# Optimization experiments

Hardware: AMD Instinct MI355X
Metric: run time of the kernel (lower is better)

## Reference

```python
import jax, jax.numpy as jnp
import numpy as np
import math

B, S, D, H, FF = 8, 1024, 1024, 16, 4096
DH = D // H
EPS = 1e-5


def _layernorm(x, g, b):
    mu = jnp.mean(x, axis=-1, keepdims=True)
    var = jnp.mean((x - mu) ** 2, axis=-1, keepdims=True)
    return (x - mu) * jax.lax.rsqrt(var + EPS) * g + b


def _gelu_tanh(x):
    c = math.sqrt(2.0 / math.pi)
    return 0.5 * x * (1.0 + jnp.tanh(c * (x + 0.044715 * x ** 3)))


def setup_inputs() -> dict:
    key = jax.random.key(0)
    ks = jax.random.split(key, 8)
    s = lambda d: 1.0 / math.sqrt(d)
    return {
        "x": jax.random.normal(ks[0], (B, S, D), jnp.float32),
        "ln1_g": jnp.ones((D,), jnp.float32),
        "ln1_b": jnp.zeros((D,), jnp.float32),
        "w_qkv": jax.random.normal(ks[1], (3 * D, D), jnp.float32) * s(D),
        "b_qkv": jax.random.normal(ks[2], (3 * D,), jnp.float32) * 0.02,
        "w_o": jax.random.normal(ks[3], (D, D), jnp.float32) * s(D),
        "b_o": jax.random.normal(ks[4], (D,), jnp.float32) * 0.02,
        "ln2_g": jnp.ones((D,), jnp.float32),
        "ln2_b": jnp.zeros((D,), jnp.float32),
        "w1": jax.random.normal(ks[5], (FF, D), jnp.float32) * s(D),
        "b1": jax.random.normal(ks[6], (FF,), jnp.float32) * 0.02,
        "w2": jax.random.normal(ks[7], (D, FF), jnp.float32) * s(FF),
        "b2": jnp.zeros((D,), jnp.float32),
    }


def reference(x, ln1_g, ln1_b, w_qkv, b_qkv, w_o, b_o, ln2_g, ln2_b, w1, b1, w2, b2):
    # --- pre-LN causal self-attention ---
    h = _layernorm(x, ln1_g, ln1_b)
    qkv = h @ w_qkv.T + b_qkv                      # [B,S,3D]
    q, k, v = jnp.split(qkv, 3, axis=-1)
    q = q.reshape(B, S, H, DH)
    k = k.reshape(B, S, H, DH)
    v = v.reshape(B, S, H, DH)
    scores = jnp.einsum("bqhd,bkhd->bhqk", q, k) / math.sqrt(DH)
    causal = jnp.triu(jnp.ones((S, S), jnp.bool_), 1)  # True above diagonal
    scores = jnp.where(causal, -jnp.inf, scores)
    attn = jax.nn.softmax(scores, axis=-1)
    o = jnp.einsum("bhqk,bkhd->bqhd", attn, v).reshape(B, S, D)
    x = x + (o @ w_o.T + b_o)
    # --- FFN ---
    h = _layernorm(x, ln2_g, ln2_b)
    h = _gelu_tanh(h @ w1.T + b1) @ w2.T + b2
    return x + h
```

## Files before the change

kernel.cpp:

```cpp
#include <hip/hip_runtime.h>
#include <math.h>


typedef __bf16 bf16_t;
typedef __bf16 bf16x4 __attribute__((ext_vector_type(4)));
typedef __bf16 bf16x8 __attribute__((ext_vector_type(8)));
typedef float f32x4 __attribute__((ext_vector_type(4)));

#define WAITVM(N) asm volatile("s_waitcnt vmcnt(" #N ")" ::: "memory")

__device__ __forceinline__ void async16(const void* g, void* l) {
    __builtin_amdgcn_global_load_lds(
        (const __attribute__((address_space(1))) void*)g,
        (__attribute__((address_space(3))) void*)l,
        16, 0, 0);
}

__device__ __forceinline__ void ln_row(const float* __restrict__ x,
                                       const float* __restrict__ g,
                                       const float* __restrict__ bb,
                                       bf16_t* __restrict__ out, int row) {
    const int tid = threadIdx.x;
    const float4 xv = *(const float4*)(x + row * 1024 + tid * 4);
    float s1 = xv.x + xv.y + xv.z + xv.w;
    float s2 = xv.x * xv.x + xv.y * xv.y + xv.z * xv.z + xv.w * xv.w;
#pragma unroll
    for (int m = 32; m >= 1; m >>= 1) {
        s1 += __shfl_xor(s1, m);
        s2 += __shfl_xor(s2, m);
    }
    __shared__ float r1[4], r2[4];
    const int wid = tid >> 6, lane = tid & 63;
    if (lane == 0) { r1[wid] = s1; r2[wid] = s2; }
    __syncthreads();
    s1 = r1[0] + r1[1] + r1[2] + r1[3];
    s2 = r2[0] + r2[1] + r2[2] + r2[3];
    const float mu = s1 * (1.0f / 1024.0f);
    const float var = s2 * (1.0f / 1024.0f) - mu * mu;
    const float rs = rsqrtf(var + 1e-5f);
    const float4 gv = *(const float4*)(g + tid * 4);
    const float4 bv = *(const float4*)(bb + tid * 4);
    bf16x4 o;
    o[0] = (bf16_t)((xv.x - mu) * rs * gv.x + bv.x);
    o[1] = (bf16_t)((xv.y - mu) * rs * gv.y + bv.y);
    o[2] = (bf16_t)((xv.z - mu) * rs * gv.z + bv.z);
    o[3] = (bf16_t)((xv.w - mu) * rs * gv.w + bv.w);
    *(bf16x4*)(out + row * 1024 + tid * 4) = o;
}

__global__ __launch_bounds__(256) void prep(
    const float* __restrict__ s0, const float* __restrict__ s1,
    const float* __restrict__ s2, const float* __restrict__ s3,
    bf16_t* __restrict__ d0, bf16_t* __restrict__ d1,
    bf16_t* __restrict__ d2, bf16_t* __restrict__ d3,
    const float* __restrict__ x, const float* __restrict__ ln1g,
    const float* __restrict__ ln1b, bf16_t* __restrict__ h) {
    if (blockIdx.x >= 12288) {
        ln_row(x, ln1g, ln1b, h, blockIdx.x - 12288);
        return;
    }
    const int g = blockIdx.x * 256 + threadIdx.x;
    const float* s;
    bf16_t* d;
    int off;
    if (g < 786432)       { s = s0; d = d0; off = g; }
    else if (g < 1048576) { s = s1; d = d1; off = g - 786432; }
    else if (g < 2097152) { s = s2; d = d2; off = g - 1048576; }
    else                  { s = s3; d = d3; off = g - 2097152; }
    const int i = off * 4;
    const float4 v = *(const float4*)(s + i);
    bf16x4 o;
    o[0] = (bf16_t)v.x; o[1] = (bf16_t)v.y; o[2] = (bf16_t)v.z; o[3] = (bf16_t)v.w;
    *(bf16x4*)(d + i) = o;
}

__global__ __launch_bounds__(256) void ln_b(const bf16_t* __restrict__ x,
                                            const float* __restrict__ g,
                                            const float* __restrict__ bb,
                                            bf16_t* __restrict__ out) {
    const int tid = threadIdx.x;
    const int row = blockIdx.x;
    const bf16x4 xb = *(const bf16x4*)(x + row * 1024 + tid * 4);
    const float x0 = (float)xb[0], x1 = (float)xb[1], x2 = (float)xb[2], x3 = (float)xb[3];
    float s1 = x0 + x1 + x2 + x3;
    float s2 = x0 * x0 + x1 * x1 + x2 * x2 + x3 * x3;
#pragma unroll
    for (int m = 32; m >= 1; m >>= 1) {
        s1 += __shfl_xor(s1, m);
        s2 += __shfl_xor(s2, m);
    }
    __shared__ float r1[4], r2[4];
    const int wid = tid >> 6, lane = tid & 63;
    if (lane == 0) { r1[wid] = s1; r2[wid] = s2; }
    __syncthreads();
    s1 = r1[0] + r1[1] + r1[2] + r1[3];
    s2 = r2[0] + r2[1] + r2[2] + r2[3];
    const float mu = s1 * (1.0f / 1024.0f);
    const float var = s2 * (1.0f / 1024.0f) - mu * mu;
    const float rs = rsqrtf(var + 1e-5f);
    const float4 gv = *(const float4*)(g + tid * 4);
    const float4 bv = *(const float4*)(bb + tid * 4);
    bf16x4 o;
    o[0] = (bf16_t)((x0 - mu) * rs * gv.x + bv.x);
    o[1] = (bf16_t)((x1 - mu) * rs * gv.y + bv.y);
    o[2] = (bf16_t)((x2 - mu) * rs * gv.z + bv.z);
    o[3] = (bf16_t)((x3 - mu) * rs * gv.w + bv.w);
    *(bf16x4*)(out + row * 1024 + tid * 4) = o;
}

template <int MODE>
__global__ __launch_bounds__(256, 2) void gemm_bt(
    const bf16_t* __restrict__ A, const bf16_t* __restrict__ W,
    const float* __restrict__ bias, const float* __restrict__ residf,
    const bf16_t* __restrict__ residb,
    bf16_t* __restrict__ outb, float* __restrict__ outf,
    bf16_t* __restrict__ vt, int N, int K) {
    __shared__ bf16_t As[128 * 64];
    __shared__ bf16_t Bs[128 * 64];
    const int tid = threadIdx.x;
    const int w = tid >> 6;
    const int lane = tid & 63;
    const int l15 = lane & 15;
    const int quad = lane >> 4;

    const int nbn = N >> 7;
    const int per = 8 * nbn;
    const int lid = blockIdx.x;
    const int bm = (lid / per) * 8 + (lid % per) % 8;
    const int bn = (lid % per) / 8;
    const int m0 = bm * 128;
    const int n0 = bn * 128;
    const int wm = (w & 1) * 64;
    const int wn = (w >> 1) * 64;

    int rr[4], so[4];
#pragma unroll
    for (int q = 0; q < 4; q++) {
        const int c = q * 256 + w * 64 + lane;
        rr[q] = c >> 3;
        so[q] = ((c & 7) ^ (rr[q] & 7)) * 8;
    }
    const bf16_t* pA[4];
    const bf16_t* pB[4];
#pragma unroll
    for (int q = 0; q < 4; q++) {
        pA[q] = A + (size_t)(m0 + rr[q]) * K + so[q];
        pB[q] = W + (size_t)(n0 + rr[q]) * K + so[q];
    }

    f32x4 acc[4][4] = {};

    for (int k0 = 0; k0 < K; k0 += 64) {
#pragma unroll
        for (int q = 0; q < 4; q++) {
            async16(pA[q], As + q * 2048 + w * 512);
            async16(pB[q], Bs + q * 2048 + w * 512);
            pA[q] += 64; pB[q] += 64;
        }
        __syncthreads();

        bf16x8 af[4][2], bfr[4][2];
#pragma unroll
        for (int i = 0; i < 4; i++) {
            const int r = wm + i * 16 + l15;
#pragma unroll
            for (int f = 0; f < 2; f++) {
                const int slot = (f * 4 + quad) ^ (r & 7);
                af[i][f] = *(const bf16x8*)(As + r * 64 + slot * 8);
            }
        }
#pragma unroll
        for (int j = 0; j < 4; j++) {
            const int r = wn + j * 16 + l15;
#pragma unroll
            for (int f = 0; f < 2; f++) {
                const int slot = (f * 4 + quad) ^ (r & 7);
                bfr[j][f] = *(const bf16x8*)(Bs + r * 64 + slot * 8);
            }
        }
#pragma unroll
        for (int i = 0; i < 4; i++)
#pragma unroll
            for (int j = 0; j < 4; j++)
#pragma unroll
                for (int f = 0; f < 2; f++)
                    acc[i][j] = __builtin_amdgcn_mfma_f32_16x16x32_bf16(
                        af[i][f], bfr[j][f], acc[i][j], 0, 0, 0);
        __syncthreads();
    }

#pragma unroll
    for (int i = 0; i < 4; i++) {
#pragma unroll
        for (int j = 0; j < 4; j++) {
            const int col = n0 + wn + j * 16 + l15;
            const float bcol = bias[col];
            const int row0 = m0 + wm + i * 16 + quad * 4;
            float v4[4];
#pragma unroll
            for (int q = 0; q < 4; q++) {
                float v = acc[i][j][q] + bcol;
                if (MODE == 1) {
                    const float u2 = -1.5957691216057308f * (v + 0.044715f * v * v * v);
                    v = v * __builtin_amdgcn_rcpf(1.0f + __expf(u2));
                }
                v4[q] = v;
            }
            if (MODE == 4) {
#pragma unroll
                for (int q = 0; q < 4; q++) {
                    const size_t idx = (size_t)(row0 + q) * N + col;
                    outb[idx] = (bf16_t)(v4[q] + residf[idx]);
                }
            } else if (MODE == 5) {
#pragma unroll
                for (int q = 0; q < 4; q++) {
                    const size_t idx = (size_t)(row0 + q) * N + col;
                    outf[idx] = v4[q] + (float)residb[idx];
                }
            } else if (MODE == 3 && col >= 2048) {
                const int bh = (row0 >> 10) * 16 + ((col - 2048) >> 6);
                const int d = (col - 2048) & 63;
                bf16x4 pk;
#pragma unroll
                for (int q = 0; q < 4; q++) pk[q] = (bf16_t)v4[q];
                *(bf16x4*)(vt + (size_t)bh * 65536 + d * 1024 + (row0 & 1023)) = pk;
            } else {
#pragma unroll
                for (int q = 0; q < 4; q++)
                    outb[(size_t)(row0 + q) * N + col] = (bf16_t)v4[q];
            }
        }
    }
}

template <int MODE>
__global__ __launch_bounds__(512, 2) void gemm8(
    const bf16_t* __restrict__ A, const bf16_t* __restrict__ W,
    const float* __restrict__ bias, bf16_t* __restrict__ outb,
    bf16_t* __restrict__ vt, int N, int K) {
    __shared__ bf16_t lds[65536];
    const int tid = threadIdx.x;
    const int w = tid >> 6, lane = tid & 63;
    const int l15 = lane & 15, quad = lane >> 4;
    const int wr = w >> 2, wc = w & 3;

    const int nbn = N >> 8;
    const int per = 8 * nbn;
    const int lid = blockIdx.x;
    const int bm = (lid / per) * 8 + (lid % per) % 8;
    const int bn = (lid % per) / 8;
    const int m0 = bm << 8, n0 = bn << 8;

    int r_[2], s_[2];
#pragma unroll
    for (int L = 0; L < 2; L++) {
        const int c = L * 512 + tid;
        r_[L] = c >> 3;
        s_[L] = ((c & 7) ^ (r_[L] & 7)) * 8;
    }
    const bf16_t* pa0[2]; const bf16_t* pa1[2];
    const bf16_t* pb0[2]; const bf16_t* pb1[2];
#pragma unroll
    for (int L = 0; L < 2; L++) {
        pa0[L] = A + (size_t)(m0 + r_[L]) * K + s_[L];
        pa1[L] = pa0[L] + (size_t)128 * K;
        pb0[L] = W + (size_t)(n0 + r_[L]) * K + s_[L];
        pb1[L] = pb0[L] + (size_t)128 * K;
    }

    int ra[8], rb[4];
#pragma unroll
    for (int i = 0; i < 8; i++) ra[i] = (i >> 2) * 128 + wr * 64 + (i & 3) * 16 + l15;
#pragma unroll
    for (int j = 0; j < 4; j++) rb[j] = (j >> 1) * 128 + wc * 32 + (j & 1) * 16 + l15;

#define FRAG(base, row, f) \
    (*(const bf16x8*)((base) + (row) * 64 + ((((f) * 4 + quad) ^ ((row) & 7)) * 8)))

    f32x4 acc[8][4] = {};
    bf16x8 af[4][2], bfr[4][2];

    async16(pa0[0], lds + w * 512);
    async16(pa0[1], lds + 4096 + w * 512);
    async16(pb0[0], lds + 16384 + w * 512);
    async16(pb0[1], lds + 16384 + 4096 + w * 512);
    async16(pb1[0], lds + 16384 + 8192 + w * 512);
    async16(pb1[1], lds + 16384 + 8192 + 4096 + w * 512);
    async16(pa1[0], lds + 8192 + w * 512);
    async16(pa1[1], lds + 8192 + 4096 + w * 512);

    const int NT = K >> 6;
    int p = 0;
    for (int t = 0; t < NT - 1; ++t, p ^= 1) {
        const bf16_t* Ab = lds + p * 32768;
        const bf16_t* Bb = Ab + 16384;
        const int q2 = p ^ 1;
        const int kn = (t + 1) << 6;
        WAITVM(4);
        __builtin_amdgcn_s_barrier();
#pragma unroll
        for (int i = 0; i < 4; i++) { af[i][0] = FRAG(Ab, ra[i], 0); af[i][1] = FRAG(Ab, ra[i], 1); }
#pragma unroll
        for (int j = 0; j < 2; j++) { bfr[j][0] = FRAG(Bb, rb[j], 0); bfr[j][1] = FRAG(Bb, rb[j], 1); }
        async16(pa0[0] + kn, lds + q2 * 32768 + w * 512);
        async16(pa0[1] + kn, lds + q2 * 32768 + 4096 + w * 512);
        __builtin_amdgcn_s_setprio(1);
#pragma unroll
        for (int i = 0; i < 4; i++)
#pragma unroll
            for (int j = 0; j < 2; j++)
#pragma unroll
                for (int f = 0; f < 2; f++)
                    acc[i][j] = __builtin_amdgcn_mfma_f32_16x16x32_bf16(af[i][f], bfr[j][f], acc[i][j], 0, 0, 0);
        __builtin_amdgcn_s_setprio(0);
        __builtin_amdgcn_s_barrier();
        WAITVM(4);
        __builtin_amdgcn_s_barrier();
#pragma unroll
        for (int j = 2; j < 4; j++) { bfr[j][0] = FRAG(Bb, rb[j], 0); bfr[j][1] = FRAG(Bb, rb[j], 1); }
        async16(pb0[0] + kn, lds + q2 * 32768 + 16384 + w * 512);
        async16(pb0[1] + kn, lds + q2 * 32768 + 16384 + 4096 + w * 512);
        __builtin_amdgcn_s_setprio(1);
#pragma unroll
        for (int i = 0; i < 4; i++)
#pragma unroll
            for (int j = 2; j < 4; j++)
#pragma unroll
                for (int f = 0; f < 2; f++)
                    acc[i][j] = __builtin_amdgcn_mfma_f32_16x16x32_bf16(af[i][f], bfr[j][f], acc[i][j], 0, 0, 0);
        __builtin_amdgcn_s_setprio(0);
        __builtin_amdgcn_s_barrier();
        WAITVM(4);
        __builtin_amdgcn_s_barrier();
#pragma unroll
        for (int i = 0; i < 4; i++) { af[i][0] = FRAG(Ab, ra[i + 4], 0); af[i][1] = FRAG(Ab, ra[i + 4], 1); }
        async16(pb1[0] + kn, lds + q2 * 32768 + 16384 + 8192 + w * 512);
        async16(pb1[1] + kn, lds + q2 * 32768 + 16384 + 8192 + 4096 + w * 512);
        __builtin_amdgcn_s_setprio(1);
#pragma unroll
        for (int i = 0; i < 4; i++)
#pragma unroll
            for (int j = 0; j < 2; j++)
#pragma unroll
                for (int f = 0; f < 2; f++)
                    acc[i + 4][j] = __builtin_amdgcn_mfma_f32_16x16x32_bf16(af[i][f], bfr[j][f], acc[i + 4][j], 0, 0, 0);
        __builtin_amdgcn_s_setprio(0);
        __builtin_amdgcn_s_barrier();
        async16(pa1[0] + kn, lds + q2 * 32768 + 8192 + w * 512);
        async16(pa1[1] + kn, lds + q2 * 32768 + 8192 + 4096 + w * 512);
        __builtin_amdgcn_s_setprio(1);
#pragma unroll
        for (int i = 0; i < 4; i++)
#pragma unroll
            for (int j = 2; j < 4; j++)
#pragma unroll
                for (int f = 0; f < 2; f++)
                    acc[i + 4][j] = __builtin_amdgcn_mfma_f32_16x16x32_bf16(af[i][f], bfr[j][f], acc[i + 4][j], 0, 0, 0);
        __builtin_amdgcn_s_setprio(0);
        __builtin_amdgcn_s_barrier();
    }
    {
        const bf16_t* Ab = lds + p * 32768;
        const bf16_t* Bb = Ab + 16384;
        WAITVM(4);
        __builtin_amdgcn_s_barrier();
#pragma unroll
        for (int i = 0; i < 4; i++) { af[i][0] = FRAG(Ab, ra[i], 0); af[i][1] = FRAG(Ab, ra[i], 1); }
#pragma unroll
        for (int j = 0; j < 2; j++) { bfr[j][0] = FRAG(Bb, rb[j], 0); bfr[j][1] = FRAG(Bb, rb[j], 1); }
        __builtin_amdgcn_s_setprio(1);
#pragma unroll
        for (int i = 0; i < 4; i++)
#pragma unroll
            for (int j = 0; j < 2; j++)
#pragma unroll
                for (int f = 0; f < 2; f++)
                    acc[i][j] = __builtin_amdgcn_mfma_f32_16x16x32_bf16(af[i][f], bfr[j][f], acc[i][j], 0, 0, 0);
        __builtin_amdgcn_s_setprio(0);
        __builtin_amdgcn_s_barrier();
        WAITVM(2);
        __builtin_amdgcn_s_barrier();
#pragma unroll
        for (int j = 2; j < 4; j++) { bfr[j][0] = FRAG(Bb, rb[j], 0); bfr[j][1] = FRAG(Bb, rb[j], 1); }
        __builtin_amdgcn_s_setprio(1);
#pragma unroll
        for (int i = 0; i < 4; i++)
#pragma unroll
            for (int j = 2; j < 4; j++)
#pragma unroll
                for (int f = 0; f < 2; f++)
                    acc[i][j] = __builtin_amdgcn_mfma_f32_16x16x32_bf16(af[i][f], bfr[j][f], acc[i][j], 0, 0, 0);
        __builtin_amdgcn_s_setprio(0);
        __builtin_amdgcn_s_barrier();
        WAITVM(0);
        __builtin_amdgcn_s_barrier();
#pragma unroll
        for (int i = 0; i < 4; i++) { af[i][0] = FRAG(Ab, ra[i + 4], 0); af[i][1] = FRAG(Ab, ra[i + 4], 1); }
        __builtin_amdgcn_s_setprio(1);
#pragma unroll
        for (int i = 0; i < 4; i++)
#pragma unroll
            for (int j = 0; j < 2; j++)
#pragma unroll
                for (int f = 0; f < 2; f++)
                    acc[i + 4][j] = __builtin_amdgcn_mfma_f32_16x16x32_bf16(af[i][f], bfr[j][f], acc[i + 4][j], 0, 0, 0);
#pragma unroll
        for (int i = 0; i < 4; i++)
#pragma unroll
            for (int j = 2; j < 4; j++)
#pragma unroll
                for (int f = 0; f < 2; f++)
                    acc[i + 4][j] = __builtin_amdgcn_mfma_f32_16x16x32_bf16(af[i][f], bfr[j][f], acc[i + 4][j], 0, 0, 0);
        __builtin_amdgcn_s_setprio(0);
    }
#undef FRAG

#pragma unroll
    for (int i = 0; i < 8; i++) {
        const int row0 = m0 + (i >> 2) * 128 + wr * 64 + (i & 3) * 16 + quad * 4;
#pragma unroll
        for (int j = 0; j < 4; j++) {
            const int col = n0 + (j >> 1) * 128 + wc * 32 + (j & 1) * 16 + l15;
            const float bcol = bias[col];
            float v4[4];
#pragma unroll
            for (int q = 0; q < 4; q++) {
                float v = acc[i][j][q] + bcol;
                if (MODE == 1) {
                    const float u2 = -1.5957691216057308f * (v + 0.044715f * v * v * v);
                    v = v * __builtin_amdgcn_rcpf(1.0f + __expf(u2));
                }
                v4[q] = v;
            }
            if (MODE == 3 && col >= 2048) {
                const int bh = (row0 >> 10) * 16 + ((col - 2048) >> 6);
                const int d = (col - 2048) & 63;
                bf16x4 pk;
#pragma unroll
                for (int q = 0; q < 4; q++) pk[q] = (bf16_t)v4[q];
                *(bf16x4*)(vt + (size_t)bh * 65536 + d * 1024 + (row0 & 1023)) = pk;
            } else {
#pragma unroll
                for (int q = 0; q < 4; q++)
                    outb[(size_t)(row0 + q) * N + col] = (bf16_t)v4[q];
            }
        }
    }
}

__global__ __launch_bounds__(512) void attn_mfma(const bf16_t* __restrict__ qkv,
                                                 const bf16_t* __restrict__ vt,
                                                 bf16_t* __restrict__ o) {
    __shared__ bf16_t Ks[4096];
    __shared__ bf16_t Vs[4096];
    __shared__ bf16_t Ps[8][32][72];
    const int tid = threadIdx.x;
    const int w = tid >> 6;
    const int lane = tid & 63;
    const int l15 = lane & 15;
    const int quad = lane >> 4;
    const int qb = blockIdx.x;
    const int bh = blockIdx.y;
    const int b = bh >> 4, h = bh & 15;

    const int qrow = b * 1024 + qb * 256 + w * 32;

    bf16x8 qf[2][2];
#pragma unroll
    for (int g = 0; g < 2; g++)
#pragma unroll
        for (int f = 0; f < 2; f++) {
            bf16x8 t = *(const bf16x8*)(qkv + (size_t)(qrow + g * 16 + l15) * 3072 + h * 64 + f * 32 + quad * 8);
#pragma unroll
            for (int e = 0; e < 8; e++) t[e] = (bf16_t)((float)t[e] * 0.125f);
            qf[g][f] = t;
        }

    f32x4 Ot[2][4] = {};
    float mrow[2] = {-3.0e38f, -3.0e38f};
    float lrow[2] = {0.0f, 0.0f};

    const int c0 = w * 64 + lane;
    const int r0 = c0 >> 3, g0 = (((c0 & 7) ^ (r0 & 7))) * 8;

    const bf16_t* kbase = qkv + (size_t)(b * 1024) * 3072 + 1024 + h * 64;
    const bf16_t* vbase = vt + (size_t)bh * 64 * 1024;

    const int ktmax = 4 * qb + 3;
    for (int kt = 0; kt <= ktmax; kt++) {
        async16(kbase + (size_t)(kt * 64 + r0) * 3072 + g0, Ks + w * 512);
        async16(vbase + (size_t)r0 * 1024 + kt * 64 + g0, Vs + w * 512);
        __syncthreads();

#pragma unroll
        for (int g = 0; g < 2; g++) {
            const int qmaxw = qb * 256 + w * 32 + g * 16 + 15;
            if (kt * 64 > qmaxw) continue;
            const int ktd = qmaxw >> 6;
            const int kbd = (2 * w + g) & 3;

            f32x4 sf[4];
#pragma unroll
            for (int kb = 0; kb < 4; kb++) {
                if (kt * 64 + kb * 16 > qmaxw) {
                    sf[kb] = (f32x4){-3.0e38f, -3.0e38f, -3.0e38f, -3.0e38f};
                    continue;
                }
                const int r = kb * 16 + l15;
                f32x4 acc = {};
#pragma unroll
                for (int f = 0; f < 2; f++) {
                    const int seg = (f * 4 + quad) ^ (r & 7);
                    const bf16x8 kf = *(const bf16x8*)(Ks + r * 64 + seg * 8);
                    acc = __builtin_amdgcn_mfma_f32_16x16x32_bf16(kf, qf[g][f], acc, 0, 0, 0);
                }
                if (kt == ktd && kb == kbd) {
#pragma unroll
                    for (int rr2 = 0; rr2 < 4; rr2++)
                        if (quad * 4 + rr2 > l15) acc[rr2] = -3.0e38f;
                }
                sf[kb] = acc;
            }

            float tmax = -3.0e38f;
#pragma unroll
            for (int kb = 0; kb < 4; kb++)
#pragma unroll
                for (int rr2 = 0; rr2 < 4; rr2++) tmax = fmaxf(tmax, sf[kb][rr2]);
            tmax = fmaxf(tmax, __shfl_xor(tmax, 16));
            tmax = fmaxf(tmax, __shfl_xor(tmax, 32));
            const float mnew = fmaxf(mrow[g], tmax);
            const float alpha = __expf(mrow[g] - mnew);
            float psum = 0.0f;
#pragma unroll
            for (int kb = 0; kb < 4; kb++) {
                bf16x4 pk;
#pragma unroll
                for (int rr2 = 0; rr2 < 4; rr2++) {
                    const float p = __expf(sf[kb][rr2] - mnew);
                    psum += p;
                    pk[rr2] = (bf16_t)p;
                }
                *(bf16x4*)(&Ps[w][g * 16 + l15][kb * 16 + quad * 4]) = pk;
            }
            psum += __shfl_xor(psum, 16);
            psum += __shfl_xor(psum, 32);
            lrow[g] = lrow[g] * alpha + psum;
            mrow[g] = mnew;
#pragma unroll
            for (int db = 0; db < 4; db++)
#pragma unroll
                for (int rr2 = 0; rr2 < 4; rr2++) Ot[g][db][rr2] *= alpha;

#pragma unroll
            for (int ks = 0; ks < 2; ks++) {
                if (kt * 64 + ks * 32 > qmaxw) break;
                const bf16x8 pf = *(const bf16x8*)(&Ps[w][g * 16 + l15][ks * 32 + quad * 8]);
#pragma unroll
                for (int db = 0; db < 4; db++) {
                    const int d = db * 16 + l15;
                    const int seg = (ks * 4 + quad) ^ (d & 7);
                    const bf16x8 vf = *(const bf16x8*)(Vs + d * 64 + seg * 8);
                    Ot[g][db] = __builtin_amdgcn_mfma_f32_16x16x32_bf16(vf, pf, Ot[g][db], 0, 0, 0);
                }
            }
        }
        __syncthreads();
    }

#pragma unroll
    for (int g = 0; g < 2; g++) {
        const float rl = 1.0f / lrow[g];
#pragma unroll
        for (int db = 0; db < 4; db++) {
            bf16x4 ov;
#pragma unroll
            for (int rr2 = 0; rr2 < 4; rr2++) ov[rr2] = (bf16_t)(Ot[g][db][rr2] * rl);
            *(bf16x4*)(o + (size_t)(qrow + g * 16 + l15) * 1024 + h * 64 + db * 16 + quad * 4) = ov;
        }
    }
}

extern "C" void kernel_launch(void* const* d_in, const int* in_sizes, int n_in,
                              void* d_out, int out_size, void* d_ws, size_t ws_size,
                              hipStream_t stream) {
    const float* x     = (const float*)d_in[0];
    const float* ln1g  = (const float*)d_in[1];
    const float* ln1b  = (const float*)d_in[2];
    const float* w_qkv = (const float*)d_in[3];
    const float* b_qkv = (const float*)d_in[4];
    const float* w_o   = (const float*)d_in[5];
    const float* b_o   = (const float*)d_in[6];
    const float* ln2g  = (const float*)d_in[7];
    const float* ln2b  = (const float*)d_in[8];
    const float* w1    = (const float*)d_in[9];
    const float* b1    = (const float*)d_in[10];
    const float* w2    = (const float*)d_in[11];
    const float* b2    = (const float*)d_in[12];
    float* out = (float*)d_out;

    char* w = (char*)d_ws;
    bf16_t* wbqkv = (bf16_t*)(w + 0);
    bf16_t* wbo   = (bf16_t*)(w + 6291456);
    bf16_t* wb1   = (bf16_t*)(w + 8388608);
    bf16_t* wb2   = (bf16_t*)(w + 16777216);
    bf16_t* h     = (bf16_t*)(w + 25165824);
    bf16_t* qkv   = (bf16_t*)(w + 41943040);
    bf16_t* ob    = (bf16_t*)(w + 92274688);
    bf16_t* x1b   = (bf16_t*)(w + 109051904);
    bf16_t* f     = (bf16_t*)(w + 142606336);
    bf16_t* vtb   = (bf16_t*)(w + 142606336);

    prep<<<20480, 256, 0, stream>>>(w_qkv, w_o, w1, w2, wbqkv, wbo, wb1, wb2,
                                    x, ln1g, ln1b, h);
    gemm8<3><<<384, 512, 0, stream>>>(h, wbqkv, b_qkv, qkv, vtb, 3072, 1024);
    attn_mfma<<<dim3(4, 128), 512, 0, stream>>>(qkv, vtb, ob);
    gemm_bt<4><<<64 * 8, 256, 0, stream>>>(ob, wbo, b_o, x, nullptr, x1b, nullptr, nullptr, 1024, 1024);
    ln_b<<<8192, 256, 0, stream>>>(x1b, ln2g, ln2b, h);
    gemm8<1><<<512, 512, 0, stream>>>(h, wb1, b1, f, nullptr, 4096, 1024);
    gemm_bt<5><<<64 * 8, 256, 0, stream>>>(f, wb2, b2, nullptr, x1b, nullptr, out, nullptr, 1024, 4096);
}
```

Measured before the change: 466.1 us.

## Issue whole next-tile prefetch upfront and remap workgroups across XCDs in gemm8

Restructures the gemm8 main loop. All eight async global-to-LDS loads for the next K tile are now issued at the start of each iteration, with a single vmcnt(0) wait at the end, replacing loads staggered across four phases with partial waits. This also removes the separate epilogue iteration. Separately, block IDs are remapped so consecutive logical tiles land on the same XCD (blockIdx & 7 striding), aiming for better L2 reuse. The trade-off is that the full wait at the end of each iteration may expose memory latency that the staggered schedule previously hid.

Measured after the change: 449.8 us. 3.5% less time.

```diff
diff --git a/kernel.cpp b/kernel.cpp
--- a/kernel.cpp
+++ b/kernel.cpp
@@ -245,11 +245,12 @@
     const int l15 = lane & 15, quad = lane >> 4;
     const int wr = w >> 2, wc = w & 3;
 
+    const int nwg = gridDim.x;
+    const int wg = (blockIdx.x & 7) * (nwg >> 3) + (blockIdx.x >> 3);
     const int nbn = N >> 8;
     const int per = 8 * nbn;
-    const int lid = blockIdx.x;
-    const int bm = (lid / per) * 8 + (lid % per) % 8;
-    const int bn = (lid % per) / 8;
+    const int bm = (wg / per) * 8 + (wg % per) % 8;
+    const int bn = (wg % per) / 8;
     const int m0 = bm << 8, n0 = bn << 8;
 
     int r_[2], s_[2];
@@ -284,27 +285,37 @@
     async16(pa0[0], lds + w * 512);
     async16(pa0[1], lds + 4096 + w * 512);
     async16(pb0[0], lds + 16384 + w * 512);
-    async16(pb0[1], lds + 16384 + 4096 + w * 512);
-    async16(pb1[0], lds + 16384 + 8192 + w * 512);
-    async16(pb1[1], lds + 16384 + 8192 + 4096 + w * 512);
+    async16(pb0[1], lds + 20480 + w * 512);
+    async16(pb1[0], lds + 24576 + w * 512);
+    async16(pb1[1], lds + 28672 + w * 512);
     async16(pa1[0], lds + 8192 + w * 512);
-    async16(pa1[1], lds + 8192 + 4096 + w * 512);
+    async16(pa1[1], lds + 12288 + w * 512);
+    WAITVM(0);
+    __builtin_amdgcn_s_barrier();
 
     const int NT = K >> 6;
     int p = 0;
-    for (int t = 0; t < NT - 1; ++t, p ^= 1) {
+    for (int t = 0; t < NT; ++t, p ^= 1) {
         const bf16_t* Ab = lds + p * 32768;
         const bf16_t* Bb = Ab + 16384;
-        const int q2 = p ^ 1;
+        bf16_t* nb = lds + (p ^ 1) * 32768;
         const int kn = (t + 1) << 6;
-        WAITVM(4);
-        __builtin_amdgcn_s_barrier();
+
 #pragma unroll
         for (int i = 0; i < 4; i++) { af[i][0] = FRAG(Ab, ra[i], 0); af[i][1] = FRAG(Ab, ra[i], 1); }
 #pragma unroll
         for (int j = 0; j < 2; j++) { bfr[j][0] = FRAG(Bb, rb[j], 0); bfr[j][1] = FRAG(Bb, rb[j], 1); }
-        async16(pa0[0] + kn, lds + q2 * 32768 + w * 512);
-        async16(pa0[1] + kn, lds + q2 * 32768 + 4096 + w * 512);
+        if (t + 1 < NT) {
+            async16(pa0[0] + kn, nb + w * 512);
+            async16(pa0[1] + kn, nb + 4096 + w * 512);
+            async16(pb0[0] + kn, nb + 16384 + w * 512);
+            async16(pb0[1] + kn, nb + 20480 + w * 512);
+            async16(pb1[0] + kn, nb + 24576 + w * 512);
+            async16(pb1[1] + kn, nb + 28672 + w * 512);
+            async16(pa1[0] + kn, nb + 8192 + w * 512);
+            async16(pa1[1] + kn, nb + 12288 + w * 512);
+        }
+        __builtin_amdgcn_s_barrier();
         __builtin_amdgcn_s_setprio(1);
 #pragma unroll
         for (int i = 0; i < 4; i++)
@@ -315,12 +326,10 @@
                     acc[i][j] = __builtin_amdgcn_mfma_f32_16x16x32_bf16(af[i][f], bfr[j][f], acc[i][j], 0, 0, 0);
         __builtin_amdgcn_s_setprio(0);
         __builtin_amdgcn_s_barrier();
-        WAITVM(4);
-        __builtin_amdgcn_s_barrier();
+
 #pragma unroll
         for (int j = 2; j < 4; j++) { bfr[j][0] = FRAG(Bb, rb[j], 0); bfr[j][1] = FRAG(Bb, rb[j], 1); }
-        async16(pb0[0] + kn, lds + q2 * 32768 + 16384 + w * 512);
-        async16(pb0[1] + kn, lds + q2 * 32768 + 16384 + 4096 + w * 512);
+        __builtin_amdgcn_s_barrier();
         __builtin_amdgcn_s_setprio(1);
 #pragma unroll
         for (int i = 0; i < 4; i++)
@@ -331,12 +340,10 @@
                     acc[i][j] = __builtin_amdgcn_mfma_f32_16x16x32_bf16(af[i][f], bfr[j][f], acc[i][j], 0, 0, 0);
         __builtin_amdgcn_s_setprio(0);
         __builtin_amdgcn_s_barrier();
-        WAITVM(4);
-        __builtin_amdgcn_s_barrier();
+
 #pragma unroll
         for (int i = 0; i < 4; i++) { af[i][0] = FRAG(Ab, ra[i + 4], 0); af[i][1] = FRAG(Ab, ra[i + 4], 1); }
-        async16(pb1[0] + kn, lds + q2 * 32768 + 16384 + 8192 + w * 512);
-        async16(pb1[1] + kn, lds + q2 * 32768 + 16384 + 8192 + 4096 + w * 512);
+        __builtin_amdgcn_s_barrier();
         __builtin_amdgcn_s_setprio(1);
 #pragma unroll
         for (int i = 0; i < 4; i++)
@@ -347,8 +354,7 @@
                     acc[i + 4][j] = __builtin_amdgcn_mfma_f32_16x16x32_bf16(af[i][f], bfr[j][f], acc[i + 4][j], 0, 0, 0);
         __builtin_amdgcn_s_setprio(0);
         __builtin_amdgcn_s_barrier();
-        async16(pa1[0] + kn, lds + q2 * 32768 + 8192 + w * 512);
-        async16(pa1[1] + kn, lds + q2 * 32768 + 8192 + 4096 + w * 512);
+
         __builtin_amdgcn_s_setprio(1);
 #pragma unroll
         for (int i = 0; i < 4; i++)
@@ -358,61 +364,8 @@
                 for (int f = 0; f < 2; f++)
                     acc[i + 4][j] = __builtin_amdgcn_mfma_f32_16x16x32_bf16(af[i][f], bfr[j][f], acc[i + 4][j], 0, 0, 0);
         __builtin_amdgcn_s_setprio(0);
-        __builtin_amdgcn_s_barrier();
-    }
-    {
-        const bf16_t* Ab = lds + p * 32768;
-        const bf16_t* Bb = Ab + 16384;
-        WAITVM(4);
-        __builtin_amdgcn_s_barrier();
-#pragma unroll
-        for (int i = 0; i < 4; i++) { af[i][0] = FRAG(Ab, ra[i], 0); af[i][1] = FRAG(Ab, ra[i], 1); }
-#pragma unroll
-        for (int j = 0; j < 2; j++) { bfr[j][0] = FRAG(Bb, rb[j], 0); bfr[j][1] = FRAG(Bb, rb[j], 1); }
-        __builtin_amdgcn_s_setprio(1);
-#pragma unroll
-        for (int i = 0; i < 4; i++)
-#pragma unroll
-            for (int j = 0; j < 2; j++)
-#pragma unroll
-                for (int f = 0; f < 2; f++)
-                    acc[i][j] = __builtin_amdgcn_mfma_f32_16x16x32_bf16(af[i][f], bfr[j][f], acc[i][j], 0, 0, 0);
-        __builtin_amdgcn_s_setprio(0);
-        __builtin_amdgcn_s_barrier();
-        WAITVM(2);
-        __builtin_amdgcn_s_barrier();
-#pragma unroll
-        for (int j = 2; j < 4; j++) { bfr[j][0] = FRAG(Bb, rb[j], 0); bfr[j][1] = FRAG(Bb, rb[j], 1); }
-        __builtin_amdgcn_s_setprio(1);
-#pragma unroll
-        for (int i = 0; i < 4; i++)
-#pragma unroll
-            for (int j = 2; j < 4; j++)
-#pragma unroll
-                for (int f = 0; f < 2; f++)
-                    acc[i][j] = __builtin_amdgcn_mfma_f32_16x16x32_bf16(af[i][f], bfr[j][f], acc[i][j], 0, 0, 0);
-        __builtin_amdgcn_s_setprio(0);
-        __builtin_amdgcn_s_barrier();
         WAITVM(0);
         __builtin_amdgcn_s_barrier();
-#pragma unroll
-        for (int i = 0; i < 4; i++) { af[i][0] = FRAG(Ab, ra[i + 4], 0); af[i][1] = FRAG(Ab, ra[i + 4], 1); }
-        __builtin_amdgcn_s_setprio(1);
-#pragma unroll
-        for (int i = 0; i < 4; i++)
-#pragma unroll
-            for (int j = 0; j < 2; j++)
-#pragma unroll
-                for (int f = 0; f < 2; f++)
-                    acc[i + 4][j] = __builtin_amdgcn_mfma_f32_16x16x32_bf16(af[i][f], bfr[j][f], acc[i + 4][j], 0, 0, 0);
-#pragma unroll
-        for (int i = 0; i < 4; i++)
-#pragma unroll
-            for (int j = 2; j < 4; j++)
-#pragma unroll
-                for (int f = 0; f < 2; f++)
-                    acc[i + 4][j] = __builtin_amdgcn_mfma_f32_16x16x32_bf16(af[i][f], bfr[j][f], acc[i + 4][j], 0, 0, 0);
-        __builtin_amdgcn_s_setprio(0);
     }
 #undef FRAG
 
```
